# Optimization experiments

Measured on AMD Instinct MI355X. Metric: run time of the kernel, lower is better.

Reference implementation:

```python
import jax, jax.numpy as jnp
import numpy as np

B, S, D = 2, 2048, 1024
H, DK = 16, 64
DFF = 4096
WINDOW = 128
GLOBAL = 16
EPS = 1e-5


def _layer_norm(x, g, b):
    mu = jnp.mean(x, axis=-1, keepdims=True)
    var = jnp.var(x, axis=-1, keepdims=True)
    return (x - mu) * jax.lax.rsqrt(var + EPS) * g + b


def setup_inputs() -> dict:
    key = jax.random.key(0)
    ks = jax.random.split(key, 12)
    s = 0.02
    inp = {
        "x": jax.random.normal(ks[0], (B, S, D), dtype=jnp.float32),
        "Wq": jax.random.normal(ks[1], (D, D), jnp.float32) * s,
        "bq": jnp.zeros((D,), jnp.float32),
        "Wk": jax.random.normal(ks[2], (D, D), jnp.float32) * s,
        "bk": jnp.zeros((D,), jnp.float32),
        "Wv": jax.random.normal(ks[3], (D, D), jnp.float32) * s,
        "bv": jnp.zeros((D,), jnp.float32),
        "Wo": jax.random.normal(ks[4], (D, D), jnp.float32) * s,
        "bo": jnp.zeros((D,), jnp.float32),
        "ln1_g": jnp.ones((D,), jnp.float32),
        "ln1_b": jnp.zeros((D,), jnp.float32),
        "W1": jax.random.normal(ks[5], (D, DFF), jnp.float32) * s,
        "b1": jnp.zeros((DFF,), jnp.float32),
        "W2": jax.random.normal(ks[6], (DFF, D), jnp.float32) * s,
        "b2": jnp.zeros((D,), jnp.float32),
        "ln2_g": jnp.ones((D,), jnp.float32),
        "ln2_b": jnp.zeros((D,), jnp.float32),
    }
    return inp


def _local_global_mask(seq_len):
    # token i attends to j iff |i-j| <= WINDOW, or i < GLOBAL, or j < GLOBAL
    i = jnp.arange(seq_len)[:, None]
    j = jnp.arange(seq_len)[None, :]
    m = jnp.abs(i - j) <= WINDOW
    m = m | (i < GLOBAL) | (j < GLOBAL)
    return m  # [S, S] bool


def reference(x, Wq, bq, Wk, bk, Wv, bv, Wo, bo, ln1_g, ln1_b,
              W1, b1, W2, b2, ln2_g, ln2_b):
    # --- self-attention sublayer (pre-norm residual) ---
    xn = _layer_norm(x, ln1_g, ln1_b)
    q = (xn @ Wq + bq).reshape(B, S, H, DK).transpose(0, 2, 1, 3)  # [B,H,S,DK]
    k = (xn @ Wk + bk).reshape(B, S, H, DK).transpose(0, 2, 1, 3)
    v = (xn @ Wv + bv).reshape(B, S, H, DK).transpose(0, 2, 1, 3)

    scores = jnp.einsum('bhqd,bhkd->bhqk', q, k) / jnp.sqrt(jnp.float32(DK))
    mask = _local_global_mask(S)  # [S,S]
    scores = jnp.where(mask[None, None], scores, jnp.float32(-jnp.inf))
    attn = jax.nn.softmax(scores, axis=-1)
    out = jnp.einsum('bhqk,bhkd->bhqd', attn, v)
    out = out.transpose(0, 2, 1, 3).reshape(B, S, D)
    out = out @ Wo + bo
    x = x + out

    # --- feed-forward sublayer (pre-norm residual) ---
    xn2 = _layer_norm(x, ln2_g, ln2_b)
    h = jax.nn.gelu(xn2 @ W1 + b1, approximate=False)
    ff = h @ W2 + b2
    x = x + ff
    return x
```

## Files before the change

kernel.cpp:

```cpp
#include <hip/hip_runtime.h>
#include <stdint.h>


typedef unsigned short u16;
typedef unsigned int   u32;
typedef __attribute__((ext_vector_type(8))) short  short8;
typedef __attribute__((ext_vector_type(4))) float  f32x4;

#define S_LEN   2048
#define D_MODEL 1024
#define ROWS    4096

__device__ __forceinline__ float bf2f(u16 u) {
  union { u32 i; float f; } v; v.i = ((u32)u) << 16; return v.f;
}
__device__ __forceinline__ float bflo(u32 u) {
  union { u32 i; float f; } v; v.i = u << 16; return v.f;
}
__device__ __forceinline__ float bfhi(u32 u) {
  union { u32 i; float f; } v; v.i = u & 0xffff0000u; return v.f;
}
__device__ __forceinline__ u16 f2bf(float f) {
  union { float f; u32 i; } v; v.f = f;
  u32 r = v.i + 0x7fffu + ((v.i >> 16) & 1u);
  return (u16)(r >> 16);
}

__device__ __forceinline__ void gld_lds16(const u16* g, u16* l) {
  __attribute__((address_space(3))) u32* lp =
      reinterpret_cast<__attribute__((address_space(3))) u32*>(
          reinterpret_cast<uintptr_t>(l));
  const __attribute__((address_space(1))) u32* gp =
      reinterpret_cast<const __attribute__((address_space(1))) u32*>(
          reinterpret_cast<uintptr_t>(g));
  __builtin_amdgcn_global_load_lds(gp, lp, 16, 0, 0);
}


template <int EPI, int OUTF>
__global__ __launch_bounds__(256) void gemm_bt(
    const u16* __restrict__ A, const u16* __restrict__ Bt,
    const float* __restrict__ bias, const float* res,
    u16* Cb, float* Cf, int M, int N, int K)
{
  __shared__ __attribute__((aligned(16))) u16 As[2][128 * 32];
  __shared__ __attribute__((aligned(16))) u16 Bs[2][128 * 32];
  const int tid  = threadIdx.x;
  const int wave = tid >> 6;
  const int lane = tid & 63;
  const int bm = blockIdx.y * 128;
  const int bn = blockIdx.x * 128;
  const int wr = (wave >> 1) * 64;
  const int wc = (wave & 1) * 64;
  const int lm = lane & 15;
  const int kq = lane >> 4;

  f32x4 acc[4][4];
#pragma unroll
  for (int i = 0; i < 4; ++i)
#pragma unroll
    for (int j = 0; j < 4; ++j) acc[i][j] = (f32x4){0.f, 0.f, 0.f, 0.f};

  const int srow = wave * 16 + (lane >> 2);
  const int kg   = (((lane & 3) - (srow >> 1)) & 3) * 8;
  const u16* gA = A  + (size_t)(bm + srow) * K + kg;
  const u16* gB = Bt + (size_t)(bn + srow) * K + kg;
  const int wb = (wave * 16) * 32;

  gld_lds16(gA, &As[0][wb]);
  gld_lds16(gA + (size_t)64 * K, &As[0][wb + 64 * 32]);
  gld_lds16(gB, &Bs[0][wb]);
  gld_lds16(gB + (size_t)64 * K, &Bs[0][wb + 64 * 32]);

  int buf = 0;
  for (int k0 = 0; k0 < K; k0 += 32, buf ^= 1) {
    __syncthreads();
    const int kn = k0 + 32;
    if (kn < K) {
      gld_lds16(gA + kn, &As[buf ^ 1][wb]);
      gld_lds16(gA + (size_t)64 * K + kn, &As[buf ^ 1][wb + 64 * 32]);
      gld_lds16(gB + kn, &Bs[buf ^ 1][wb]);
      gld_lds16(gB + (size_t)64 * K + kn, &Bs[buf ^ 1][wb + 64 * 32]);
    }

    short8 af[4], bfv[4];
#pragma unroll
    for (int ti = 0; ti < 4; ++ti) {
      const int Ra = wr + ti * 16 + lm;
      af[ti] = *(const short8*)&As[buf][Ra * 32 + (((kq + (Ra >> 1)) & 3) * 8)];
    }
#pragma unroll
    for (int tj = 0; tj < 4; ++tj) {
      const int Rb = wc + tj * 16 + lm;
      bfv[tj] = *(const short8*)&Bs[buf][Rb * 32 + (((kq + (Rb >> 1)) & 3) * 8)];
    }
#pragma unroll
    for (int ti = 0; ti < 4; ++ti)
#pragma unroll
      for (int tj = 0; tj < 4; ++tj)
        acc[ti][tj] = __builtin_amdgcn_mfma_f32_16x16x32_bf16(
            af[ti], bfv[tj], acc[ti][tj], 0, 0, 0);
  }

  const int r0 = (lane >> 4) * 4;
#pragma unroll
  for (int ti = 0; ti < 4; ++ti) {
#pragma unroll
    for (int r = 0; r < 4; ++r) {
      const int grow = bm + wr + ti * 16 + r0 + r;
#pragma unroll
      for (int tj = 0; tj < 4; ++tj) {
        const int gcol = bn + wc + tj * 16 + lm;
        const size_t idx = (size_t)grow * N + gcol;
        float v = acc[ti][tj][r] + bias[gcol];
        if (EPI == 1) v = 0.5f * v * (1.0f + erff(v * 0.70710678118654752f));
        if (OUTF) Cf[idx] = v;
        else      Cb[idx] = f2bf(v);
      }
    }
  }
}

__global__ __launch_bounds__(256) void gemm_sp(
    const u16* __restrict__ A, const u16* __restrict__ Bt,
    u16* __restrict__ P0, u16* __restrict__ P1,
    int M, int N, int K, int KH)
{
  __shared__ __attribute__((aligned(16))) u16 As[2][128 * 32];
  __shared__ __attribute__((aligned(16))) u16 Bs[2][128 * 32];
  const int tid  = threadIdx.x;
  const int wave = tid >> 6;
  const int lane = tid & 63;
  const int bm = blockIdx.y * 128;
  const int bn = blockIdx.x * 128;
  const int kz = blockIdx.z;
  u16* P = kz ? P1 : P0;
  const int wr = (wave >> 1) * 64;
  const int wc = (wave & 1) * 64;
  const int lm = lane & 15;
  const int kq = lane >> 4;

  f32x4 acc[4][4];
#pragma unroll
  for (int i = 0; i < 4; ++i)
#pragma unroll
    for (int j = 0; j < 4; ++j) acc[i][j] = (f32x4){0.f, 0.f, 0.f, 0.f};

  const int srow = wave * 16 + (lane >> 2);
  const int kg   = (((lane & 3) - (srow >> 1)) & 3) * 8;
  const u16* gA = A  + (size_t)(bm + srow) * K + kz * KH + kg;
  const u16* gB = Bt + (size_t)(bn + srow) * K + kz * KH + kg;
  const int wb = (wave * 16) * 32;

  gld_lds16(gA, &As[0][wb]);
  gld_lds16(gA + (size_t)64 * K, &As[0][wb + 64 * 32]);
  gld_lds16(gB, &Bs[0][wb]);
  gld_lds16(gB + (size_t)64 * K, &Bs[0][wb + 64 * 32]);

  int buf = 0;
  for (int k0 = 0; k0 < KH; k0 += 32, buf ^= 1) {
    __syncthreads();
    const int kn = k0 + 32;
    if (kn < KH) {
      gld_lds16(gA + kn, &As[buf ^ 1][wb]);
      gld_lds16(gA + (size_t)64 * K + kn, &As[buf ^ 1][wb + 64 * 32]);
      gld_lds16(gB + kn, &Bs[buf ^ 1][wb]);
      gld_lds16(gB + (size_t)64 * K + kn, &Bs[buf ^ 1][wb + 64 * 32]);
    }

    short8 af[4], bfv[4];
#pragma unroll
    for (int ti = 0; ti < 4; ++ti) {
      const int Ra = wr + ti * 16 + lm;
      af[ti] = *(const short8*)&As[buf][Ra * 32 + (((kq + (Ra >> 1)) & 3) * 8)];
    }
#pragma unroll
    for (int tj = 0; tj < 4; ++tj) {
      const int Rb = wc + tj * 16 + lm;
      bfv[tj] = *(const short8*)&Bs[buf][Rb * 32 + (((kq + (Rb >> 1)) & 3) * 8)];
    }
#pragma unroll
    for (int ti = 0; ti < 4; ++ti)
#pragma unroll
      for (int tj = 0; tj < 4; ++tj)
        acc[ti][tj] = __builtin_amdgcn_mfma_f32_16x16x32_bf16(
            af[ti], bfv[tj], acc[ti][tj], 0, 0, 0);
  }

  const int r0 = (lane >> 4) * 4;
#pragma unroll
  for (int ti = 0; ti < 4; ++ti) {
#pragma unroll
    for (int r = 0; r < 4; ++r) {
      const int grow = bm + wr + ti * 16 + r0 + r;
#pragma unroll
      for (int tj = 0; tj < 4; ++tj) {
        const int gcol = bn + wc + tj * 16 + lm;
        P[(size_t)grow * N + gcol] = f2bf(acc[ti][tj][r]);
      }
    }
  }
}

__global__ __launch_bounds__(256) void reduce2(
    const u16* __restrict__ P0, const u16* __restrict__ P1,
    const float* __restrict__ bias, const float* res, float* out)
{
  const size_t base = ((size_t)blockIdx.x * 256 + threadIdx.x) * 8;
  const int col = (int)(base & 1023);
  uint4 p0 = *(const uint4*)(P0 + base);
  uint4 p1 = *(const uint4*)(P1 + base);
  float4 b0 = *(const float4*)(bias + col);
  float4 b1 = *(const float4*)(bias + col + 4);
  float4 r0 = *(const float4*)(res + base);
  float4 r1 = *(const float4*)(res + base + 4);
  float4 o0, o1;
  o0.x = bflo(p0.x) + bflo(p1.x) + b0.x + r0.x;
  o0.y = bfhi(p0.x) + bfhi(p1.x) + b0.y + r0.y;
  o0.z = bflo(p0.y) + bflo(p1.y) + b0.z + r0.z;
  o0.w = bfhi(p0.y) + bfhi(p1.y) + b0.w + r0.w;
  o1.x = bflo(p0.z) + bflo(p1.z) + b1.x + r1.x;
  o1.y = bfhi(p0.z) + bfhi(p1.z) + b1.y + r1.y;
  o1.z = bflo(p0.w) + bflo(p1.w) + b1.z + r1.z;
  o1.w = bfhi(p0.w) + bfhi(p1.w) + b1.w + r1.w;
  *(float4*)(out + base) = o0;
  *(float4*)(out + base + 4) = o1;
}

__global__ __launch_bounds__(256) void ln_kernel(
    const float* __restrict__ x, const float* __restrict__ g,
    const float* __restrict__ b, u16* __restrict__ o)
{
  const int row = blockIdx.x;
  const int t = threadIdx.x;
  float4 v = *(const float4*)(x + (size_t)row * D_MODEL + t * 4);
  float s  = v.x + v.y + v.z + v.w;
  float ss = v.x * v.x + v.y * v.y + v.z * v.z + v.w * v.w;
#pragma unroll
  for (int off = 32; off > 0; off >>= 1) {
    s  += __shfl_down(s, off);
    ss += __shfl_down(ss, off);
  }
  __shared__ float sm[4], ssm[4], stat[2];
  if ((t & 63) == 0) { sm[t >> 6] = s; ssm[t >> 6] = ss; }
  __syncthreads();
  if (t == 0) {
    float S = sm[0] + sm[1] + sm[2] + sm[3];
    float SS = ssm[0] + ssm[1] + ssm[2] + ssm[3];
    float mu = S * (1.0f / 1024.0f);
    float var = SS * (1.0f / 1024.0f) - mu * mu;
    stat[0] = mu;
    stat[1] = rsqrtf(fmaxf(var, 0.0f) + 1e-5f);
  }
  __syncthreads();
  const float mu = stat[0], rstd = stat[1];
  float4 gg = *(const float4*)(g + t * 4);
  float4 bb = *(const float4*)(b + t * 4);
  u16 o0 = f2bf((v.x - mu) * rstd * gg.x + bb.x);
  u16 o1 = f2bf((v.y - mu) * rstd * gg.y + bb.y);
  u16 o2 = f2bf((v.z - mu) * rstd * gg.z + bb.z);
  u16 o3 = f2bf((v.w - mu) * rstd * gg.w + bb.w);
  uint2 w;
  w.x = (u32)o0 | ((u32)o1 << 16);
  w.y = (u32)o2 | ((u32)o3 << 16);
  *(uint2*)(o + (size_t)row * D_MODEL + t * 4) = w;
}

__global__ __launch_bounds__(256) void attn_band(
    const u16* __restrict__ qkv, u16* __restrict__ out)
{
  const int t    = threadIdx.x;
  const int w    = t >> 6;
  const int lane = t & 63;
  const int m    = lane & 15;
  const int quad = lane >> 4;
  const int bh   = blockIdx.y;
  const int b    = bh >> 4, h = bh & 15;
  const int i0   = blockIdx.x * 64;
  const size_t bb = (size_t)b * S_LEN;

  __shared__ __attribute__((aligned(16))) u16 Ks[32 * 72];
  __shared__ __attribute__((aligned(16))) u16 Vt[64 * 40];
  __shared__ __attribute__((aligned(16))) u16 Ps[4][16 * 40];

  const u16* qrow = qkv + (bb + i0 + 16 * w + m) * 3072 + h * 64;
  const short8 aq0 = *(const short8*)(qrow + quad * 8);
  const short8 aq1 = *(const short8*)(qrow + 32 + quad * 8);

  f32x4 Ov[4];
#pragma unroll
  for (int td = 0; td < 4; ++td) Ov[td] = (f32x4){0.f, 0.f, 0.f, 0.f};
  float mP[4] = {-1e30f, -1e30f, -1e30f, -1e30f};
  float lS[4] = {0.f, 0.f, 0.f, 0.f};

  const int iB = i0 + 16 * w + quad * 4;

  const int lo = max(32, i0 - 128);
  const int hi = min(S_LEN, i0 + 192);
  const int nChunks = 1 + (hi - lo) / 32;

  const int skr = t >> 3;
  const int skc = (t & 7) * 8;

  for (int c = 0; c < nChunks; ++c) {
    const int j0 = (c == 0) ? 0 : lo + (c - 1) * 32;
    __syncthreads();
    {
      const u16* src = qkv + (bb + j0 + skr) * 3072 + 1024 + h * 64 + skc;
      uint4 kk = *(const uint4*)src;
      uint4 vv = *(const uint4*)(src + 1024);
      *(uint4*)&Ks[skr * 72 + skc] = kk;
      const u16 vs[8] = {
        (u16)(vv.x & 0xffffu), (u16)(vv.x >> 16),
        (u16)(vv.y & 0xffffu), (u16)(vv.y >> 16),
        (u16)(vv.z & 0xffffu), (u16)(vv.z >> 16),
        (u16)(vv.w & 0xffffu), (u16)(vv.w >> 16)};
#pragma unroll
      for (int i = 0; i < 8; ++i) Vt[(skc + i) * 40 + skr] = vs[i];
    }
    __syncthreads();

    const short8 b00 = *(const short8*)&Ks[m * 72 + quad * 8];
    const short8 b01 = *(const short8*)&Ks[m * 72 + 32 + quad * 8];
    const short8 b10 = *(const short8*)&Ks[(16 + m) * 72 + quad * 8];
    const short8 b11 = *(const short8*)&Ks[(16 + m) * 72 + 32 + quad * 8];
    f32x4 s0 = (f32x4){0.f, 0.f, 0.f, 0.f};
    f32x4 s1 = (f32x4){0.f, 0.f, 0.f, 0.f};
    s0 = __builtin_amdgcn_mfma_f32_16x16x32_bf16(aq0, b00, s0, 0, 0, 0);
    s0 = __builtin_amdgcn_mfma_f32_16x16x32_bf16(aq1, b01, s0, 0, 0, 0);
    s1 = __builtin_amdgcn_mfma_f32_16x16x32_bf16(aq0, b10, s1, 0, 0, 0);
    s1 = __builtin_amdgcn_mfma_f32_16x16x32_bf16(aq1, b11, s1, 0, 0, 0);

    const int jA = j0 + m, jB = j0 + 16 + m;
#pragma unroll
    for (int r = 0; r < 4; ++r) {
      const int iG = iB + r;
      const int da = iG - jA, db = iG - jB;
      s0[r] = ((jA < 16) || (da >= -128 && da <= 128)) ? s0[r] * 0.125f : -1e30f;
      s1[r] = ((jB < 16) || (db >= -128 && db <= 128)) ? s1[r] * 0.125f : -1e30f;
    }

    float al[4];
#pragma unroll
    for (int r = 0; r < 4; ++r) {
      float mx = fmaxf(s0[r], s1[r]);
      mx = fmaxf(mx, __shfl_xor(mx, 1, 16));
      mx = fmaxf(mx, __shfl_xor(mx, 2, 16));
      mx = fmaxf(mx, __shfl_xor(mx, 4, 16));
      mx = fmaxf(mx, __shfl_xor(mx, 8, 16));
      const float mn = fmaxf(mP[r], mx);
      al[r] = __expf(mP[r] - mn);
      mP[r] = mn;
      const float p0 = __expf(s0[r] - mn);
      const float p1 = __expf(s1[r] - mn);
      float ps = p0 + p1;
      ps += __shfl_xor(ps, 1, 16);
      ps += __shfl_xor(ps, 2, 16);
      ps += __shfl_xor(ps, 4, 16);
      ps += __shfl_xor(ps, 8, 16);
      lS[r] = lS[r] * al[r] + ps;
      Ps[w][(quad * 4 + r) * 40 + m]      = f2bf(p0);
      Ps[w][(quad * 4 + r) * 40 + 16 + m] = f2bf(p1);
    }
#pragma unroll
    for (int td = 0; td < 4; ++td)
#pragma unroll
      for (int r = 0; r < 4; ++r) Ov[td][r] *= al[r];

    const short8 pa = *(const short8*)&Ps[w][m * 40 + quad * 8];
#pragma unroll
    for (int td = 0; td < 4; ++td) {
      const short8 bv = *(const short8*)&Vt[(td * 16 + m) * 40 + quad * 8];
      Ov[td] = __builtin_amdgcn_mfma_f32_16x16x32_bf16(pa, bv, Ov[td], 0, 0, 0);
    }
  }

  if (i0 + 16 * w >= 16) {
    float inv[4];
#pragma unroll
    for (int r = 0; r < 4; ++r) inv[r] = 1.0f / lS[r];
#pragma unroll
    for (int td = 0; td < 4; ++td)
#pragma unroll
      for (int r = 0; r < 4; ++r)
        out[(bb + iB + r) * 1024 + h * 64 + td * 16 + m] =
            f2bf(Ov[td][r] * inv[r]);
  }
}

__global__ __launch_bounds__(256) void attn_gpart(
    const u16* __restrict__ qkv, float* __restrict__ Obuf,
    float* __restrict__ mbuf, float* __restrict__ lbuf)
{
  const int t    = threadIdx.x;
  const int w    = t >> 6;
  const int lane = t & 63;
  const int m    = lane & 15;
  const int quad = lane >> 4;
  const int kb   = blockIdx.x;
  const int bh   = blockIdx.y;
  const int b    = bh >> 4, h = bh & 15;
  const size_t bb = (size_t)b * S_LEN;

  __shared__ __attribute__((aligned(16))) u16 Ks[4][32 * 72];
  __shared__ __attribute__((aligned(16))) u16 Vt[4][64 * 40];
  __shared__ __attribute__((aligned(16))) u16 Ps[4][16 * 40];

  const u16* qrow = qkv + (bb + m) * 3072 + h * 64;
  const short8 aq0 = *(const short8*)(qrow + quad * 8);
  const short8 aq1 = *(const short8*)(qrow + 32 + quad * 8);

  f32x4 Ov[4];
#pragma unroll
  for (int td = 0; td < 4; ++td) Ov[td] = (f32x4){0.f, 0.f, 0.f, 0.f};
  float mP[4] = {-1e30f, -1e30f, -1e30f, -1e30f};
  float lS[4] = {0.f, 0.f, 0.f, 0.f};

  const int srow = lane >> 1;
  const int sd   = (lane & 1) * 32;

  for (int c = 0; c < 2; ++c) {
    const int j0 = kb * 256 + w * 64 + c * 32;
    {
      const u16* src = qkv + (bb + j0 + srow) * 3072 + 1024 + h * 64 + sd;
      uint4 k0 = *(const uint4*)(src);
      uint4 k1 = *(const uint4*)(src + 8);
      uint4 k2 = *(const uint4*)(src + 16);
      uint4 k3 = *(const uint4*)(src + 24);
      *(uint4*)&Ks[w][srow * 72 + sd]      = k0;
      *(uint4*)&Ks[w][srow * 72 + sd + 8]  = k1;
      *(uint4*)&Ks[w][srow * 72 + sd + 16] = k2;
      *(uint4*)&Ks[w][srow * 72 + sd + 24] = k3;
#pragma unroll
      for (int q4 = 0; q4 < 4; ++q4) {
        uint4 vv = *(const uint4*)(src + 1024 + q4 * 8);
        const u16 vs[8] = {
          (u16)(vv.x & 0xffffu), (u16)(vv.x >> 16),
          (u16)(vv.y & 0xffffu), (u16)(vv.y >> 16),
          (u16)(vv.z & 0xffffu), (u16)(vv.z >> 16),
          (u16)(vv.w & 0xffffu), (u16)(vv.w >> 16)};
#pragma unroll
        for (int i = 0; i < 8; ++i)
          Vt[w][(sd + q4 * 8 + i) * 40 + srow] = vs[i];
      }
    }

    const short8 b00 = *(const short8*)&Ks[w][m * 72 + quad * 8];
    const short8 b01 = *(const short8*)&Ks[w][m * 72 + 32 + quad * 8];
    const short8 b10 = *(const short8*)&Ks[w][(16 + m) * 72 + quad * 8];
    const short8 b11 = *(const short8*)&Ks[w][(16 + m) * 72 + 32 + quad * 8];
    f32x4 s0 = (f32x4){0.f, 0.f, 0.f, 0.f};
    f32x4 s1 = (f32x4){0.f, 0.f, 0.f, 0.f};
    s0 = __builtin_amdgcn_mfma_f32_16x16x32_bf16(aq0, b00, s0, 0, 0, 0);
    s0 = __builtin_amdgcn_mfma_f32_16x16x32_bf16(aq1, b01, s0, 0, 0, 0);
    s1 = __builtin_amdgcn_mfma_f32_16x16x32_bf16(aq0, b10, s1, 0, 0, 0);
    s1 = __builtin_amdgcn_mfma_f32_16x16x32_bf16(aq1, b11, s1, 0, 0, 0);

    float al[4];
#pragma unroll
    for (int r = 0; r < 4; ++r) {
      const float v0 = s0[r] * 0.125f, v1 = s1[r] * 0.125f;
      float mx = fmaxf(v0, v1);
      mx = fmaxf(mx, __shfl_xor(mx, 1, 16));
      mx = fmaxf(mx, __shfl_xor(mx, 2, 16));
      mx = fmaxf(mx, __shfl_xor(mx, 4, 16));
      mx = fmaxf(mx, __shfl_xor(mx, 8, 16));
      const float mn = fmaxf(mP[r], mx);
      al[r] = __expf(mP[r] - mn);
      mP[r] = mn;
      const float p0 = __expf(v0 - mn);
      const float p1 = __expf(v1 - mn);
      float ps = p0 + p1;
      ps += __shfl_xor(ps, 1, 16);
      ps += __shfl_xor(ps, 2, 16);
      ps += __shfl_xor(ps, 4, 16);
      ps += __shfl_xor(ps, 8, 16);
      lS[r] = lS[r] * al[r] + ps;
      Ps[w][(quad * 4 + r) * 40 + m]      = f2bf(p0);
      Ps[w][(quad * 4 + r) * 40 + 16 + m] = f2bf(p1);
    }
#pragma unroll
    for (int td = 0; td < 4; ++td)
#pragma unroll
      for (int r = 0; r < 4; ++r) Ov[td][r] *= al[r];

    const short8 pa = *(const short8*)&Ps[w][m * 40 + quad * 8];
#pragma unroll
    for (int td = 0; td < 4; ++td) {
      const short8 bv = *(const short8*)&Vt[w][(td * 16 + m) * 40 + quad * 8];
      Ov[td] = __builtin_amdgcn_mfma_f32_16x16x32_bf16(pa, bv, Ov[td], 0, 0, 0);
    }
  }

  const int p = kb * 4 + w;
  const size_t ob = ((size_t)(bh * 32 + p)) * 16 * 64;
#pragma unroll
  for (int td = 0; td < 4; ++td)
#pragma unroll
    for (int r = 0; r < 4; ++r)
      Obuf[ob + (size_t)(quad * 4 + r) * 64 + td * 16 + m] = Ov[td][r];
  if (m == 0) {
    const int mb = (bh * 32 + p) * 16;
#pragma unroll
    for (int r = 0; r < 4; ++r) {
      mbuf[mb + quad * 4 + r] = mP[r];
      lbuf[mb + quad * 4 + r] = lS[r];
    }
  }
}

__global__ __launch_bounds__(256) void attn_gcombine(
    const float* __restrict__ Obuf, const float* __restrict__ mbuf,
    const float* __restrict__ lbuf, u16* __restrict__ out)
{
  const int bh = blockIdx.x;
  const int b  = bh >> 4, h = bh & 15;
  const int t  = threadIdx.x;
  const int q  = t >> 4;
  const int d0 = (t & 15) * 4;
  const int mb = bh * 32 * 16;

  float mv[32];
  float M = -1e30f;
#pragma unroll
  for (int p = 0; p < 32; ++p) {
    mv[p] = mbuf[mb + p * 16 + q];
    M = fmaxf(M, mv[p]);
  }
  float L = 0.f;
  float4 acc = {0.f, 0.f, 0.f, 0.f};
#pragma unroll
  for (int p = 0; p < 32; ++p) {
    const float wp = __expf(mv[p] - M);
    L += lbuf[mb + p * 16 + q] * wp;
    float4 o = *(const float4*)&Obuf[(((size_t)(bh * 32 + p)) * 16 + q) * 64 + d0];
    acc.x += wp * o.x; acc.y += wp * o.y;
    acc.z += wp * o.z; acc.w += wp * o.w;
  }
  const float inv = 1.0f / L;
  uint2 wv;
  wv.x = (u32)f2bf(acc.x * inv) | ((u32)f2bf(acc.y * inv) << 16);
  wv.y = (u32)f2bf(acc.z * inv) | ((u32)f2bf(acc.w * inv) << 16);
  *(uint2*)(out + ((size_t)b * S_LEN + q) * 1024 + h * 64 + d0) = wv;
}

__global__ __launch_bounds__(256) void prep_all(
    const float* __restrict__ Wq, const float* __restrict__ Wk,
    const float* __restrict__ Wv, const float* __restrict__ Wo,
    const float* __restrict__ W1, const float* __restrict__ W2,
    const float* __restrict__ bq, const float* __restrict__ bk,
    const float* __restrict__ bv,
    u16* __restrict__ WQKVT, u16* __restrict__ WOT,
    u16* __restrict__ W1T, u16* __restrict__ W2T,
    float* __restrict__ BQKV)
{
  const int gb = blockIdx.x;
  const int t = threadIdx.x;
  if (gb >= 3072) {
    const int i = (gb - 3072) * 256 + t;
    if (i < 1024) BQKV[i] = bq[i];
    else if (i < 2048) BQKV[i] = bk[i - 1024];
    else BQKV[i] = bv[i - 2048];
    return;
  }
  const float* in; u16* outp; int R, Cc, bx, by;
  if (gb < 1024) {
    const int seg = gb >> 8, local = gb & 255;
    bx = local & 15; by = local >> 4; R = 1024; Cc = 1024;
    in   = (seg == 0) ? Wq : (seg == 1) ? Wk : (seg == 2) ? Wv : Wo;
    outp = (seg < 3) ? WQKVT + (size_t)seg * 1024 * 1024 : WOT;
  } else if (gb < 2048) {
    const int local = gb - 1024;
    bx = local & 63; by = local >> 6; R = 1024; Cc = 4096;
    in = W1; outp = W1T;
  } else {
    const int local = gb - 2048;
    bx = local & 15; by = local >> 4; R = 4096; Cc = 1024;
    in = W2; outp = W2T;
  }

  __shared__ u16 tile[64][65];
  const int tr = by * 64, tc = bx * 64;
  const int lr = t >> 2, lc0 = (t & 3) * 16;
  const float* src = in + (size_t)(tr + lr) * Cc + tc + lc0;
  float4 a0 = *(const float4*)(src);
  float4 a1 = *(const float4*)(src + 4);
  float4 a2 = *(const float4*)(src + 8);
  float4 a3 = *(const float4*)(src + 12);
  const float vals[16] = {a0.x, a0.y, a0.z, a0.w, a1.x, a1.y, a1.z, a1.w,
                          a2.x, a2.y, a2.z, a2.w, a3.x, a3.y, a3.z, a3.w};
#pragma unroll
  for (int q = 0; q < 16; ++q) tile[lr][lc0 + q] = f2bf(vals[q]);
  __syncthreads();
  u16* dst = outp + (size_t)(tc + lr) * R + tr + lc0;
  u32 w[8];
#pragma unroll
  for (int q = 0; q < 8; ++q)
    w[q] = (u32)tile[lc0 + 2 * q][lr] | ((u32)tile[lc0 + 2 * q + 1][lr] << 16);
  uint4 s0; s0.x = w[0]; s0.y = w[1]; s0.z = w[2]; s0.w = w[3];
  uint4 s1; s1.x = w[4]; s1.y = w[5]; s1.z = w[6]; s1.w = w[7];
  *(uint4*)dst = s0;
  *(uint4*)(dst + 8) = s1;
}

static const size_t OFF_WQKVT = 0;
static const size_t OFF_WOT   = OFF_WQKVT + (size_t)3072 * 1024 * 2;
static const size_t OFF_W1T   = OFF_WOT   + (size_t)1024 * 1024 * 2;
static const size_t OFF_W2T   = OFF_W1T   + (size_t)4096 * 1024 * 2;
static const size_t OFF_BQKV  = OFF_W2T   + (size_t)1024 * 4096 * 2;
static const size_t OFF_XN    = OFF_BQKV  + 16384;
static const size_t OFF_QKV   = OFF_XN    + (size_t)4096 * 1024 * 2;
static const size_t OFF_AO    = OFF_QKV   + (size_t)4096 * 3072 * 2;
static const size_t OFF_H     = OFF_QKV;

extern "C" void kernel_launch(void* const* d_in, const int* in_sizes, int n_in,
                              void* d_out, int out_size, void* d_ws, size_t ws_size,
                              hipStream_t stream)
{
  const float* x   = (const float*)d_in[0];
  const float* Wq  = (const float*)d_in[1];
  const float* bq  = (const float*)d_in[2];
  const float* Wk  = (const float*)d_in[3];
  const float* bk  = (const float*)d_in[4];
  const float* Wv  = (const float*)d_in[5];
  const float* bv  = (const float*)d_in[6];
  const float* Wo  = (const float*)d_in[7];
  const float* bo  = (const float*)d_in[8];
  const float* g1  = (const float*)d_in[9];
  const float* be1 = (const float*)d_in[10];
  const float* W1  = (const float*)d_in[11];
  const float* b1  = (const float*)d_in[12];
  const float* W2  = (const float*)d_in[13];
  const float* b2  = (const float*)d_in[14];
  const float* g2  = (const float*)d_in[15];
  const float* be2 = (const float*)d_in[16];
  float* outf = (float*)d_out;
  char* ws = (char*)d_ws;

  u16*   WQKVT = (u16*)(ws + OFF_WQKVT);
  u16*   WOT   = (u16*)(ws + OFF_WOT);
  u16*   W1T   = (u16*)(ws + OFF_W1T);
  u16*   W2T   = (u16*)(ws + OFF_W2T);
  float* BQKV  = (float*)(ws + OFF_BQKV);
  u16*   XN    = (u16*)(ws + OFF_XN);
  u16*   QKV   = (u16*)(ws + OFF_QKV);
  u16*   AO    = (u16*)(ws + OFF_AO);
  u16*   Hbuf  = (u16*)(ws + OFF_H);
  float* X1    = outf;
  u16* PWo0 = (u16*)(ws + OFF_QKV);
  u16* PWo1 = PWo0 + (size_t)4096 * 1024;
  u16* PW20 = (u16*)(ws + OFF_W1T);
  u16* PW21 = (u16*)(ws + OFF_XN);
  float* GO = (float*)(ws + OFF_XN);
  float* GM = GO + (size_t)32 * 32 * 16 * 64;
  float* GL = GM + 32 * 32 * 16;

  const dim3 blk(256);
  prep_all<<<dim3(3084), blk, 0, stream>>>(Wq, Wk, Wv, Wo, W1, W2, bq, bk, bv,
                                           WQKVT, WOT, W1T, W2T, BQKV);

  ln_kernel<<<dim3(ROWS), blk, 0, stream>>>(x, g1, be1, XN);
  gemm_bt<0, 0><<<dim3(24, 32), blk, 0, stream>>>(XN, WQKVT, BQKV, nullptr,
                                                  QKV, nullptr, ROWS, 3072, 1024);
  attn_band<<<dim3(32, 32), blk, 0, stream>>>(QKV, AO);
  attn_gpart<<<dim3(8, 32), blk, 0, stream>>>(QKV, GO, GM, GL);
  attn_gcombine<<<dim3(32), blk, 0, stream>>>(GO, GM, GL, AO);
  gemm_sp<<<dim3(8, 32, 2), blk, 0, stream>>>(AO, WOT, PWo0, PWo1,
                                              ROWS, 1024, 1024, 512);
  reduce2<<<dim3(2048), blk, 0, stream>>>(PWo0, PWo1, bo, x, X1);

  ln_kernel<<<dim3(ROWS), blk, 0, stream>>>(X1, g2, be2, XN);
  gemm_bt<1, 0><<<dim3(32, 32), blk, 0, stream>>>(XN, W1T, b1, nullptr,
                                                  Hbuf, nullptr, ROWS, 4096, 1024);
  gemm_sp<<<dim3(8, 32, 2), blk, 0, stream>>>(Hbuf, W2T, PW20, PW21,
                                              ROWS, 1024, 4096, 2048);
  reduce2<<<dim3(2048), blk, 0, stream>>>(PW20, PW21, b2, X1, outf);
}
```

Baseline: 364.7 us.

## Replace 128x128 GEMM with 256x256 8-wave pipelined kernel for QKV and FFN1

```diff
diff --git a/kernel.cpp b/kernel.cpp
--- a/kernel.cpp
+++ b/kernel.cpp
@@ -37,85 +37,144 @@
 }
 
 
-template <int EPI, int OUTF>
-__global__ __launch_bounds__(256) void gemm_bt(
+#define GBAR  __builtin_amdgcn_s_barrier()
+#define LGKM0 asm volatile("s_waitcnt lgkmcnt(0)" ::: "memory")
+#define VM4   asm volatile("s_waitcnt vmcnt(4)" ::: "memory")
+#define VM0   asm volatile("s_waitcnt vmcnt(0)" ::: "memory")
+
+#define STAGE_A(buf, t, hm) do {                                              \
+    gld_lds16(pA[hm][0] + (size_t)(t) * 64, &Ald[buf][0][(hm)*4096 + ldst]);  \
+    gld_lds16(pA[hm][1] + (size_t)(t) * 64, &Ald[buf][1][(hm)*4096 + ldst]);  \
+  } while (0)
+
+#define STAGE_B(buf, t, hm) do {                                              \
+    gld_lds16(pB[hm][0] + (size_t)(t) * 64, &Bld[buf][0][(hm)*4096 + ldst]);  \
+    gld_lds16(pB[hm][1] + (size_t)(t) * 64, &Bld[buf][1][(hm)*4096 + ldst]);  \
+  } while (0)
+
+#define READ_B(buf) do {                                                      \
+    _Pragma("unroll") for (int nj = 0; nj < 4; ++nj) {                        \
+      bfv[nj][0] = *(const short8*)&Bld[buf][0][brow + nj * 512];             \
+      bfv[nj][1] = *(const short8*)&Bld[buf][1][brow + nj * 512]; }           \
+  } while (0)
+
+#define READ_A(buf, q) do {                                                   \
+    af[0][0] = *(const short8*)&Ald[buf][0][arow + (2*(q)) * 512];            \
+    af[0][1] = *(const short8*)&Ald[buf][1][arow + (2*(q)) * 512];            \
+    af[1][0] = *(const short8*)&Ald[buf][0][arow + (2*(q)+1) * 512];          \
+    af[1][1] = *(const short8*)&Ald[buf][1][arow + (2*(q)+1) * 512];          \
+  } while (0)
+
+#define MFMA_Q(q) do {                                                        \
+    __builtin_amdgcn_s_setprio(1);                                            \
+    _Pragma("unroll") for (int dm = 0; dm < 2; ++dm)                          \
+    _Pragma("unroll") for (int kk = 0; kk < 2; ++kk)                          \
+    _Pragma("unroll") for (int nj = 0; nj < 4; ++nj)                          \
+      acc[2*(q)+dm][nj] = __builtin_amdgcn_mfma_f32_16x16x32_bf16(            \
+          af[dm][kk], bfv[nj][kk], acc[2*(q)+dm][nj], 0, 0, 0);               \
+    __builtin_amdgcn_s_setprio(0);                                            \
+  } while (0)
+
+#define PHASE(buf, q, STAGE_STMT, TAILWAIT) do {                              \
+    if ((q) == 0) READ_B(buf);                                                \
+    READ_A(buf, q);                                                           \
+    STAGE_STMT;                                                               \
+    GBAR;                                                                     \
+    LGKM0;                                                                    \
+    MFMA_Q(q);                                                                \
+    TAILWAIT;                                                                 \
+    GBAR;                                                                     \
+  } while (0)
+
+template <int EPI>
+__global__ __launch_bounds__(512) void gemm256(
     const u16* __restrict__ A, const u16* __restrict__ Bt,
-    const float* __restrict__ bias, const float* res,
-    u16* Cb, float* Cf, int M, int N, int K)
-{
-  __shared__ __attribute__((aligned(16))) u16 As[2][128 * 32];
-  __shared__ __attribute__((aligned(16))) u16 Bs[2][128 * 32];
+    const float* __restrict__ bias, u16* __restrict__ C,
+    int N, int K)
+{
+  __shared__ __attribute__((aligned(16))) u16 Ald[2][2][256 * 32];
+  __shared__ __attribute__((aligned(16))) u16 Bld[2][2][256 * 32];
+
   const int tid  = threadIdx.x;
-  const int wave = tid >> 6;
+  const int w    = tid >> 6;
   const int lane = tid & 63;
-  const int bm = blockIdx.y * 128;
-  const int bn = blockIdx.x * 128;
-  const int wr = (wave >> 1) * 64;
-  const int wc = (wave & 1) * 64;
-  const int lm = lane & 15;
-  const int kq = lane >> 4;
-
-  f32x4 acc[4][4];
-#pragma unroll
-  for (int i = 0; i < 4; ++i)
+  const int wm   = w >> 2;
+  const int wn   = w & 3;
+  const int lm   = lane & 15;
+  const int kq   = lane >> 4;
+  const int bm   = blockIdx.y * 256;
+  const int bn   = blockIdx.x * 256;
+
+  const int rslot = ((kq + (lm >> 1)) & 3) * 8;
+  const int arow  = (wm * 128 + lm) * 32 + rslot;
+  const int brow  = (wn * 64  + lm) * 32 + rslot;
+
+  const int gcoff = (((lane & 3) - (lane >> 3)) & 3) * 8;
+  const int srow  = w * 16 + (lane >> 2);
+  const int ldst  = w * 512;
+
+  const u16* pA[2][2];
+  const u16* pB[2][2];
+#pragma unroll
+  for (int hm = 0; hm < 2; ++hm)
+#pragma unroll
+    for (int j = 0; j < 2; ++j) {
+      pA[hm][j] = A  + (size_t)(bm + hm * 128 + srow) * K + j * 32 + gcoff;
+      pB[hm][j] = Bt + (size_t)(bn + hm * 128 + srow) * K + j * 32 + gcoff;
+    }
+
+  f32x4 acc[8][4];
+#pragma unroll
+  for (int i = 0; i < 8; ++i)
 #pragma unroll
     for (int j = 0; j < 4; ++j) acc[i][j] = (f32x4){0.f, 0.f, 0.f, 0.f};
 
-  const int srow = wave * 16 + (lane >> 2);
-  const int kg   = (((lane & 3) - (srow >> 1)) & 3) * 8;
-  const u16* gA = A  + (size_t)(bm + srow) * K + kg;
-  const u16* gB = Bt + (size_t)(bn + srow) * K + kg;
-  const int wb = (wave * 16) * 32;
-
-  gld_lds16(gA, &As[0][wb]);
-  gld_lds16(gA + (size_t)64 * K, &As[0][wb + 64 * 32]);
-  gld_lds16(gB, &Bs[0][wb]);
-  gld_lds16(gB + (size_t)64 * K, &Bs[0][wb + 64 * 32]);
-
-  int buf = 0;
-  for (int k0 = 0; k0 < K; k0 += 32, buf ^= 1) {
-    __syncthreads();
-    const int kn = k0 + 32;
-    if (kn < K) {
-      gld_lds16(gA + kn, &As[buf ^ 1][wb]);
-      gld_lds16(gA + (size_t)64 * K + kn, &As[buf ^ 1][wb + 64 * 32]);
-      gld_lds16(gB + kn, &Bs[buf ^ 1][wb]);
-      gld_lds16(gB + (size_t)64 * K + kn, &Bs[buf ^ 1][wb + 64 * 32]);
-    }
-
-    short8 af[4], bfv[4];
-#pragma unroll
-    for (int ti = 0; ti < 4; ++ti) {
-      const int Ra = wr + ti * 16 + lm;
-      af[ti] = *(const short8*)&As[buf][Ra * 32 + (((kq + (Ra >> 1)) & 3) * 8)];
-    }
-#pragma unroll
-    for (int tj = 0; tj < 4; ++tj) {
-      const int Rb = wc + tj * 16 + lm;
-      bfv[tj] = *(const short8*)&Bs[buf][Rb * 32 + (((kq + (Rb >> 1)) & 3) * 8)];
-    }
-#pragma unroll
-    for (int ti = 0; ti < 4; ++ti)
-#pragma unroll
-      for (int tj = 0; tj < 4; ++tj)
-        acc[ti][tj] = __builtin_amdgcn_mfma_f32_16x16x32_bf16(
-            af[ti], bfv[tj], acc[ti][tj], 0, 0, 0);
-  }
-
-  const int r0 = (lane >> 4) * 4;
-#pragma unroll
-  for (int ti = 0; ti < 4; ++ti) {
+  short8 af[2][2];
+  short8 bfv[4][2];
+
+  const int P = K >> 7;
+
+  STAGE_B(0, 0, 0); STAGE_B(0, 0, 1);
+  STAGE_A(0, 0, 0); STAGE_A(0, 0, 1);
+  STAGE_B(1, 1, 0); STAGE_B(1, 1, 1);
+  VM4;
+  GBAR;
+
+  for (int i = 0; i < P - 1; ++i) {
+    const int t1 = 2 * i + 1, t2 = 2 * i + 2, t3 = 2 * i + 3;
+    PHASE(0, 0, STAGE_A(1, t1, 0), );
+    PHASE(0, 1, STAGE_A(1, t1, 1), );
+    PHASE(0, 2, STAGE_B(0, t2, 0), );
+    PHASE(0, 3, STAGE_B(0, t2, 1), VM4);
+    PHASE(1, 0, STAGE_A(0, t2, 0), );
+    PHASE(1, 1, STAGE_A(0, t2, 1), );
+    PHASE(1, 2, STAGE_B(1, t3, 0), );
+    PHASE(1, 3, STAGE_B(1, t3, 1), VM4);
+  }
+  {
+    const int t1 = 2 * P - 1;
+    PHASE(0, 0, STAGE_A(1, t1, 0), );
+    PHASE(0, 1, STAGE_A(1, t1, 1), );
+    PHASE(0, 2, , );
+    PHASE(0, 3, , VM0);
+    PHASE(1, 0, , );
+    PHASE(1, 1, , );
+    PHASE(1, 2, , );
+    PHASE(1, 3, , );
+  }
+
+  const int r0 = kq * 4;
+#pragma unroll
+  for (int mi = 0; mi < 8; ++mi) {
 #pragma unroll
     for (int r = 0; r < 4; ++r) {
-      const int grow = bm + wr + ti * 16 + r0 + r;
-#pragma unroll
-      for (int tj = 0; tj < 4; ++tj) {
-        const int gcol = bn + wc + tj * 16 + lm;
-        const size_t idx = (size_t)grow * N + gcol;
-        float v = acc[ti][tj][r] + bias[gcol];
+      const int grow = bm + wm * 128 + mi * 16 + r0 + r;
+#pragma unroll
+      for (int nj = 0; nj < 4; ++nj) {
+        const int gcol = bn + wn * 64 + nj * 16 + lm;
+        float v = acc[mi][nj][r] + bias[gcol];
         if (EPI == 1) v = 0.5f * v * (1.0f + erff(v * 0.70710678118654752f));
-        if (OUTF) Cf[idx] = v;
-        else      Cb[idx] = f2bf(v);
+        C[(size_t)grow * N + gcol] = f2bf(v);
       }
     }
   }
@@ -660,8 +719,8 @@
                                            WQKVT, WOT, W1T, W2T, BQKV);
 
   ln_kernel<<<dim3(ROWS), blk, 0, stream>>>(x, g1, be1, XN);
-  gemm_bt<0, 0><<<dim3(24, 32), blk, 0, stream>>>(XN, WQKVT, BQKV, nullptr,
-                                                  QKV, nullptr, ROWS, 3072, 1024);
+  gemm256<0><<<dim3(12, 16), dim3(512), 0, stream>>>(XN, WQKVT, BQKV, QKV,
+                                                     3072, 1024);
   attn_band<<<dim3(32, 32), blk, 0, stream>>>(QKV, AO);
   attn_gpart<<<dim3(8, 32), blk, 0, stream>>>(QKV, GO, GM, GL);
   attn_gcombine<<<dim3(32), blk, 0, stream>>>(GO, GM, GL, AO);
@@ -670,8 +729,8 @@
   reduce2<<<dim3(2048), blk, 0, stream>>>(PWo0, PWo1, bo, x, X1);
 
   ln_kernel<<<dim3(ROWS), blk, 0, stream>>>(X1, g2, be2, XN);
-  gemm_bt<1, 0><<<dim3(32, 32), blk, 0, stream>>>(XN, W1T, b1, nullptr,
-                                                  Hbuf, nullptr, ROWS, 4096, 1024);
+  gemm256<1><<<dim3(16, 16), dim3(512), 0, stream>>>(XN, W1T, b1, Hbuf,
+                                                     4096, 1024);
   gemm_sp<<<dim3(8, 32, 2), blk, 0, stream>>>(Hbuf, W2T, PW20, PW21,
                                               ROWS, 1024, 4096, 2048);
   reduce2<<<dim3(2048), blk, 0, stream>>>(PW20, PW21, b2, X1, outf);
```

Measured after the change: 351.1 us. -3.7%, faster.
